# Performance work log

Hardware: AMD Instinct MI355X
Metric: run time of the kernel (lower is better)

Reference implementation:

```python
import jax, jax.numpy as jnp
import numpy as np

B, T, N = 32, 512, 16
C, V, D, H, L = 150, 832, 512, 512, 5  # chord vocab, note vocab, embed dim, hidden, layers


def setup_inputs() -> dict:
    key = jax.random.key(0)
    ks = jax.random.split(key, 16)
    s = 0.05
    note = jax.random.randint(ks[0], (B, T, N), 0, V)
    chord = jax.random.randint(ks[1], (B, T), 0, C)
    chord_table = jax.random.normal(ks[2], (C, D), jnp.float32) * s
    note_table = jax.random.normal(ks[3], (V, D), jnp.float32) * s
    # GRU layer 0 (input = 2*D), layers 1..L-1 (input = H), gate order r,z,n like torch
    w_ih0 = jax.random.normal(ks[4], (3 * H, 2 * D), jnp.float32) * s
    w_hh0 = jax.random.normal(ks[5], (3 * H, H), jnp.float32) * s
    b_ih0 = jax.random.normal(ks[6], (3 * H,), jnp.float32) * s
    b_hh0 = jax.random.normal(ks[7], (3 * H,), jnp.float32) * s
    w_ih_r = jax.random.normal(ks[8], (L - 1, 3 * H, H), jnp.float32) * s
    w_hh_r = jax.random.normal(ks[9], (L - 1, 3 * H, H), jnp.float32) * s
    b_ih_r = jax.random.normal(ks[10], (L - 1, 3 * H), jnp.float32) * s
    b_hh_r = jax.random.normal(ks[11], (L - 1, 3 * H), jnp.float32) * s
    fc_w = jax.random.normal(ks[12], (C, H), jnp.float32) * s
    fc_b = jax.random.normal(ks[13], (C,), jnp.float32) * s
    return dict(note=note, chord=chord, chord_table=chord_table, note_table=note_table,
                w_ih0=w_ih0, w_hh0=w_hh0, b_ih0=b_ih0, b_hh0=b_hh0,
                w_ih_r=w_ih_r, w_hh_r=w_hh_r, b_ih_r=b_ih_r, b_hh_r=b_hh_r,
                fc_w=fc_w, fc_b=fc_b)


def _gru_layer(x, wih, whh, bih, bhh):
    # x: [B, T, in] -> [B, T, H], torch GRU cell math (gate order r,z,n)
    xp = jnp.einsum('bti,gi->btg', x, wih) + bih          # precompute input proj [B,T,3H]
    xp = jnp.swapaxes(xp, 0, 1)                            # [T,B,3H]
    h0 = jnp.zeros((x.shape[0], whh.shape[1]), x.dtype)

    def step(h, xpt):
        gh = h @ whh.T + bhh
        xr, xz, xn = jnp.split(xpt, 3, axis=-1)
        hr, hz, hn = jnp.split(gh, 3, axis=-1)
        r = jax.nn.sigmoid(xr + hr)
        z = jax.nn.sigmoid(xz + hz)
        n = jnp.tanh(xn + r * hn)
        h_new = (1.0 - z) * n + z * h
        return h_new, h_new

    _, ys = jax.lax.scan(step, h0, xp)
    return jnp.swapaxes(ys, 0, 1)                          # [B,T,H]


def _forward(note, chord, chord_table, note_table, w_ih0, w_hh0, b_ih0, b_hh0,
             w_ih_r, w_hh_r, b_ih_r, b_hh_r, fc_w, fc_b):
    # padding_idx=0: zero row 0 of both tables (also blocks its gradient)
    ct = chord_table.at[0].set(0.0)
    nt = note_table.at[0].set(0.0)
    chord_emb = ct[chord]                                   # [B,T,D]
    # ragged mean over notes before first zero; mask[k]=1 iff no zero in note[...,:k+1]
    mask = jnp.cumprod((note != 0).astype(chord_table.dtype), axis=-1)  # [B,T,N]
    emb = nt[note]                                          # [B,T,N,D]
    cnt = jnp.maximum(mask.sum(-1), 1.0)                    # zero_index==0 case -> mean of zero row
    note_emb = jnp.einsum('btnd,btn->btd', emb, mask) / cnt[..., None]
    x = jnp.concatenate([chord_emb, note_emb], axis=-1)     # [B,T,2D]
    x = _gru_layer(x, w_ih0, w_hh0, b_ih0, b_hh0)
    for l in range(w_ih_r.shape[0]):
        x = _gru_layer(x, w_ih_r[l], w_hh_r[l], b_ih_r[l], b_hh_r[l])
    return x @ fc_w.T + fc_b                                # [B,T,C]


def reference(note, chord, chord_table, note_table, w_ih0, w_hh0, b_ih0, b_hh0,
              w_ih_r, w_hh_r, b_ih_r, b_hh_r, fc_w, fc_b):
    return _forward(note, chord, chord_table, note_table, w_ih0, w_hh0, b_ih0, b_hh0,
                    w_ih_r, w_hh_r, b_ih_r, b_hh_r, fc_w, fc_b)
```

## Files before the change

kernel.cpp:

```cpp
#include <hip/hip_runtime.h>
#include <hip/hip_bf16.h>

#define B_   32
#define T_   512
#define NN_  16
#define CV_  150
#define D_   512
#define H_   512
#define BT_  16384
#define K0_  1024
#define G3H_ 1536
#define SUBS_ 32
#define NBF_ 160
#define WSZ_ 49152

using bf16x8 = __attribute__((ext_vector_type(8))) short;
using f32x4  = __attribute__((ext_vector_type(4))) float;
using u32x4  = __attribute__((ext_vector_type(4))) unsigned int;
typedef unsigned long long u64;

__device__ __forceinline__ unsigned short f2bf(float f){
  unsigned int u = __builtin_bit_cast(unsigned int, f);
  u += 0x7fffu + ((u >> 16) & 1u);
  return (unsigned short)(u >> 16);
}

__device__ __forceinline__ void store8(unsigned short* p, f32x4 a, f32x4 b){
  union { unsigned short us[8]; u32x4 v; } u;
  u.us[0]=f2bf(a[0]); u.us[1]=f2bf(a[1]); u.us[2]=f2bf(a[2]); u.us[3]=f2bf(a[3]);
  u.us[4]=f2bf(b[0]); u.us[5]=f2bf(b[1]); u.us[6]=f2bf(b[2]); u.us[7]=f2bf(b[3]);
  *(u32x4*)p = u.v;
}

__device__ __forceinline__ u64 ld_coh_u64(const u64* p){
  return __hip_atomic_load(p, __ATOMIC_RELAXED, __HIP_MEMORY_SCOPE_AGENT);
}
__device__ __forceinline__ void st_coh_u32(void* p, unsigned int v){
  __hip_atomic_store((unsigned int*)p, v, __ATOMIC_RELAXED, __HIP_MEMORY_SCOPE_AGENT);
}
__device__ __forceinline__ void st_flag(int* p, int v){
  __hip_atomic_store(p, v, __ATOMIC_RELAXED, __HIP_MEMORY_SCOPE_AGENT);
}
__device__ __forceinline__ int ld_flag(const int* p){
  return __hip_atomic_load(p, __ATOMIC_RELAXED, __HIP_MEMORY_SCOPE_AGENT);
}

__global__ void convert_bf16(const float* __restrict__ src,
                             unsigned short* __restrict__ dst, int n){
  int i = blockIdx.x * 256 + threadIdx.x;
  if (i < n) dst[i] = f2bf(src[i]);
}

__global__ void prep_wfrag(const float* __restrict__ whh0,
                           const float* __restrict__ whhr,
                           const float* __restrict__ wihr,
                           unsigned short* __restrict__ wsw, int total){
  int idx = blockIdx.x * 256 + threadIdx.x;
  if (idx >= total) return;
  int pos = idx & 511;
  int lam = pos >> 3, e = pos & 7;
  int fr  = idx >> 9;
  int ks  = fr & 31;
  int g   = (fr >> 5) % 3;
  int blk = fr / 96;
  int sub = blk & 31, l = blk >> 5;
  int row = g * 512 + sub * 16 + (lam & 15);
  int k   = (ks & 15) * 32 + (lam >> 4) * 8 + e;
  float v;
  if (l == 0) v = (ks < 16) ? whh0[(size_t)row * H_ + k] : 0.f;
  else {
    const float* w = (ks < 16) ? (whhr + (size_t)(l - 1) * G3H_ * H_)
                               : (wihr + (size_t)(l - 1) * G3H_ * H_);
    v = w[(size_t)row * H_ + k];
  }
  wsw[idx] = f2bf(v);
}

__global__ void prep_bias(const float* __restrict__ bhh0,
                          const float* __restrict__ bihr,
                          const float* __restrict__ bhhr,
                          float* __restrict__ bias_sw, int total){
  int idx = blockIdx.x * 256 + threadIdx.x;
  if (idx >= total) return;
  int q = idx & 3, u = (idx >> 2) & 15, sub = (idx >> 6) & 31, l = idx >> 11;
  int j = sub * 16 + u;
  float v;
  if (l == 0){
    v = (q == 0) ? bhh0[j] : (q == 1) ? bhh0[512 + j] : (q == 2) ? 0.f : bhh0[1024 + j];
  } else {
    const float* bi = bihr + (size_t)(l - 1) * G3H_;
    const float* bh = bhhr + (size_t)(l - 1) * G3H_;
    v = (q == 0) ? bi[j] + bh[j]
      : (q == 1) ? bi[512 + j] + bh[512 + j]
      : (q == 2) ? bi[1024 + j] : bh[1024 + j];
  }
  bias_sw[idx] = v;
}

__global__ __launch_bounds__(64) void emb_kernel(
    const int* __restrict__ note, const int* __restrict__ chord,
    const float* __restrict__ ctab, const float* __restrict__ ntab,
    unsigned short* __restrict__ x0){
  const int bt = blockIdx.x;
  const int tid = threadIdx.x;
  __shared__ int sn[NN_];
  if (tid < NN_) sn[tid] = note[bt * NN_ + tid];
  __syncthreads();
  float alive = 1.f, cnt = 0.f;
  float msk[NN_];
  #pragma unroll
  for (int k = 0; k < NN_; ++k){ if (sn[k] == 0) alive = 0.f; msk[k] = alive; cnt += alive; }
  const float inv = 1.f / fmaxf(cnt, 1.f);
  const int ch = chord[bt];
  const int d0 = tid * 8;
  f32x4 c0 = {0.f,0.f,0.f,0.f}, c1 = {0.f,0.f,0.f,0.f};
  if (ch != 0){
    const float* cp = ctab + (size_t)ch * D_ + d0;
    c0 = *(const f32x4*)cp; c1 = *(const f32x4*)(cp + 4);
  }
  f32x4 s0 = {0.f,0.f,0.f,0.f}, s1 = {0.f,0.f,0.f,0.f};
  #pragma unroll
  for (int k = 0; k < NN_; ++k){
    if (msk[k] != 0.f){
      const float* np = ntab + (size_t)sn[k] * D_ + d0;
      s0 += *(const f32x4*)np;
      s1 += *(const f32x4*)(np + 4);
    }
  }
  s0 *= inv; s1 *= inv;
  unsigned short* o = x0 + (size_t)bt * K0_ + d0;
  store8(o, c0, c1);
  store8(o + D_, s0, s1);
}

__global__ __launch_bounds__(256) void gemm_bt(
    const unsigned short* __restrict__ X, const unsigned short* __restrict__ W,
    const float* __restrict__ bias, float* __restrict__ Y,
    int M, int N, int K, int wmode){
  const int lane = threadIdx.x & 63;
  const int wave = threadIdx.x >> 6;
  const int l15 = lane & 15, kq4 = lane >> 4;
  const int m_frag = blockIdx.y * 64 + wave * 16 + l15;
  const int n_base = blockIdx.x * 64;
  f32x4 acc[4] = {{0.f,0.f,0.f,0.f},{0.f,0.f,0.f,0.f},{0.f,0.f,0.f,0.f},{0.f,0.f,0.f,0.f}};
  const unsigned short* xptr = X + (size_t)m_frag * K + kq4 * 8;
  const unsigned short* wptr[4];
  #pragma unroll
  for (int i = 0; i < 4; ++i){
    int n = n_base + i * 16 + l15;
    if (n >= N) n = N - 1;
    wptr[i] = W + (size_t)n * K + kq4 * 8;
  }
  for (int k0 = 0; k0 < K; k0 += 32){
    bf16x8 a = *(const bf16x8*)(xptr + k0);
    #pragma unroll
    for (int i = 0; i < 4; ++i){
      bf16x8 b = *(const bf16x8*)(wptr[i] + k0);
      acc[i] = __builtin_amdgcn_mfma_f32_16x16x32_bf16(a, b, acc[i], 0, 0, 0);
    }
  }
  const int mrow = blockIdx.y * 64 + wave * 16 + kq4 * 4;
  #pragma unroll
  for (int i = 0; i < 4; ++i){
    int n = n_base + i * 16 + l15;
    if (n < N){
      float bv = bias[n];
      #pragma unroll
      for (int r = 0; r < 4; ++r){
        int m = mrow + r;
        float v = acc[i][r] + bv;
        if (wmode == 0) Y[(size_t)m * N + n] = v;
        else            Y[((size_t)(m & (T_-1)) * N + n) * B_ + (m >> 9)] = v;
      }
    }
  }
}

__global__ __launch_bounds__(256, 1) void gru_fused(
    const float* __restrict__ xp, const unsigned short* __restrict__ wsw,
    const float* __restrict__ bias_sw, unsigned short* __restrict__ hT,
    unsigned short* __restrict__ xT, unsigned short* __restrict__ xout,
    int* __restrict__ flags){
  __shared__ unsigned short w_s[96 * 512];
  __shared__ unsigned short stage_s[32 * 512];
  __shared__ float p_s[4][2][16][16];
  __shared__ float bias_s[64];

  const int tid = threadIdx.x;
  const int blk = blockIdx.x;
  const int l   = blk >> 5;
  const int sub = blk & 31;
  const int lane = tid & 63, wave = tid >> 6;
  const int l15 = lane & 15, l4 = lane >> 4;
  const int myn = wave >> 1;
  const bool rzw = (wave & 1) == 0;

  {
    const u32x4* src = (const u32x4*)(wsw + (size_t)blk * WSZ_);
    u32x4* dst = (u32x4*)w_s;
    #pragma unroll
    for (int i = 0; i < 24; ++i) dst[tid + 256 * i] = src[tid + 256 * i];
  }
  if (tid < 64) bias_s[tid] = bias_sw[blk * 64 + tid];

  const int cb = tid & 31;
  const int cj = (tid >> 5) * 2;
  const int jg = sub * 16 + cj;
  float hres0 = 0.f, hres1 = 0.f;

  unsigned short* hTl = hT + (size_t)l * (2 * 32 * 512);
  unsigned short* xTw = xT + (size_t)l * (4 * 32 * 512);
  const unsigned short* xTr = xT + (size_t)(l - 1) * (4 * 32 * 512);

  auto stage = [&](const unsigned short* __restrict__ src){
    u64 lo[8], hi[8];
    #pragma unroll
    for (int i = 0; i < 8; ++i){
      int c = tid + 256 * i;
      int f = c >> 6, lam = c & 63;
      int b = ((f >> 4) << 4) | (lam & 15);
      int k = ((f & 15) << 5) | ((lam >> 4) << 3);
      const u64* sp = (const u64*)(src + b * 512 + k);
      lo[i] = ld_coh_u64(sp);
      hi[i] = ld_coh_u64(sp + 1);
    }
    #pragma unroll
    for (int i = 0; i < 8; ++i){
      int c = tid + 256 * i;
      *(u64*)&stage_s[c * 8]     = lo[i];
      *(u64*)&stage_s[c * 8 + 4] = hi[i];
    }
  };

  __syncthreads();

  for (int s = 0; s < T_ + 4; ++s){
    const int t = s - l;
    const bool act = (t >= 0) && (t < T_);
    if (act){
      f32x4 accA = {0.f,0.f,0.f,0.f}, accB = {0.f,0.f,0.f,0.f};
      stage(hTl + (size_t)(t & 1) * (32 * 512));
      __syncthreads();
      #pragma unroll
      for (int ks = 0; ks < 16; ++ks){
        bf16x8 b = *(const bf16x8*)&stage_s[((myn << 4) + ks) * 512 + lane * 8];
        if (rzw){
          bf16x8 a0 = *(const bf16x8*)&w_s[(0 * 32 + ks) * 512 + lane * 8];
          bf16x8 a1 = *(const bf16x8*)&w_s[(1 * 32 + ks) * 512 + lane * 8];
          accA = __builtin_amdgcn_mfma_f32_16x16x32_bf16(a0, b, accA, 0, 0, 0);
          accB = __builtin_amdgcn_mfma_f32_16x16x32_bf16(a1, b, accB, 0, 0, 0);
        } else {
          bf16x8 a2 = *(const bf16x8*)&w_s[(2 * 32 + ks) * 512 + lane * 8];
          accA = __builtin_amdgcn_mfma_f32_16x16x32_bf16(a2, b, accA, 0, 0, 0);
        }
      }
      float er = 0.f, ez = 0.f, en = 0.f, er1 = 0.f, ez1 = 0.f, en1 = 0.f;
      if (l > 0){
        __syncthreads();
        stage(xTr + (size_t)(t & 3) * (32 * 512));
        __syncthreads();
        #pragma unroll
        for (int ks = 0; ks < 16; ++ks){
          bf16x8 b = *(const bf16x8*)&stage_s[((myn << 4) + ks) * 512 + lane * 8];
          if (rzw){
            bf16x8 a0 = *(const bf16x8*)&w_s[(0 * 32 + 16 + ks) * 512 + lane * 8];
            bf16x8 a1 = *(const bf16x8*)&w_s[(1 * 32 + 16 + ks) * 512 + lane * 8];
            accA = __builtin_amdgcn_mfma_f32_16x16x32_bf16(a0, b, accA, 0, 0, 0);
            accB = __builtin_amdgcn_mfma_f32_16x16x32_bf16(a1, b, accB, 0, 0, 0);
          } else {
            bf16x8 a2 = *(const bf16x8*)&w_s[(2 * 32 + 16 + ks) * 512 + lane * 8];
            accB = __builtin_amdgcn_mfma_f32_16x16x32_bf16(a2, b, accB, 0, 0, 0);
          }
        }
      } else {
        const float* xb = xp + (size_t)t * (G3H_ * B_) + cb;
        er  = xb[(size_t)(0 * H_ + jg) * B_];  er1 = xb[(size_t)(0 * H_ + jg + 1) * B_];
        ez  = xb[(size_t)(1 * H_ + jg) * B_];  ez1 = xb[(size_t)(1 * H_ + jg + 1) * B_];
        en  = xb[(size_t)(2 * H_ + jg) * B_];  en1 = xb[(size_t)(2 * H_ + jg + 1) * B_];
      }
      #pragma unroll
      for (int r = 0; r < 4; ++r){
        int u = l4 * 4 + r;
        if (rzw){ p_s[0][myn][u][l15] = accA[r]; p_s[1][myn][u][l15] = accB[r]; }
        else    { p_s[2][myn][u][l15] = accA[r]; p_s[3][myn][u][l15] = accB[r]; }
      }
      __syncthreads();
      {
        const int nt = cb >> 4, bc = cb & 15;
        const float* bs = bias_s + cj * 4;
        float rp0 = p_s[0][nt][cj][bc],     rp1 = p_s[0][nt][cj + 1][bc];
        float zp0 = p_s[1][nt][cj][bc],     zp1 = p_s[1][nt][cj + 1][bc];
        float hp0 = p_s[2][nt][cj][bc],     hp1 = p_s[2][nt][cj + 1][bc];
        float xq0 = p_s[3][nt][cj][bc],     xq1 = p_s[3][nt][cj + 1][bc];
        float r0 = 1.f / (1.f + __expf(-(rp0 + er  + bs[0])));
        float r1 = 1.f / (1.f + __expf(-(rp1 + er1 + bs[4])));
        float z0 = 1.f / (1.f + __expf(-(zp0 + ez  + bs[1])));
        float z1 = 1.f / (1.f + __expf(-(zp1 + ez1 + bs[5])));
        float nx0 = (l > 0) ? (xq0 + bs[2]) : en;
        float nx1 = (l > 0) ? (xq1 + bs[6]) : en1;
        float e0 = __expf(2.f * (nx0 + r0 * (hp0 + bs[3])));
        float e1 = __expf(2.f * (nx1 + r1 * (hp1 + bs[7])));
        float n0 = (e0 - 1.f) / (e0 + 1.f);
        float n1 = (e1 - 1.f) / (e1 + 1.f);
        float h0 = (1.f - z0) * n0 + z0 * hres0; hres0 = h0;
        float h1 = (1.f - z1) * n1 + z1 * hres1; hres1 = h1;
        unsigned int pk = (unsigned int)f2bf(h0) | ((unsigned int)f2bf(h1) << 16);
        st_coh_u32(hTl + (size_t)((t + 1) & 1) * (32 * 512) + cb * 512 + jg, pk);
        if (l < 4) st_coh_u32(xTw + (size_t)(t & 3) * (32 * 512) + cb * 512 + jg, pk);
        else *(unsigned int*)&xout[((size_t)cb * T_ + t) * H_ + jg] = pk;
      }
    }
    __syncthreads();
    if (tid == 0) st_flag(&flags[blk], s + 1);
    if (tid < 64){
      const int tgt = s + 1;
      while (true){
        int v0 = ld_flag(&flags[tid]);
        int v1 = ld_flag(&flags[tid + 64]);
        int v2 = (tid < 32) ? ld_flag(&flags[tid + 128]) : tgt;
        if (__all(v0 >= tgt && v1 >= tgt && v2 >= tgt)) break;
      }
    }
    __syncthreads();
  }
}

extern "C" void kernel_launch(void* const* d_in, const int* in_sizes, int n_in,
                              void* d_out, int out_size, void* d_ws, size_t ws_size,
                              hipStream_t stream){
  (void)in_sizes; (void)n_in; (void)out_size; (void)ws_size;
  const int*   note  = (const int*)d_in[0];
  const int*   chord = (const int*)d_in[1];
  const float* ctab  = (const float*)d_in[2];
  const float* ntab  = (const float*)d_in[3];
  const float* wih0  = (const float*)d_in[4];
  const float* whh0  = (const float*)d_in[5];
  const float* bih0  = (const float*)d_in[6];
  const float* bhh0  = (const float*)d_in[7];
  const float* wihr  = (const float*)d_in[8];
  const float* whhr  = (const float*)d_in[9];
  const float* bihr  = (const float*)d_in[10];
  const float* bhhr  = (const float*)d_in[11];
  const float* fcw   = (const float*)d_in[12];
  const float* fcb   = (const float*)d_in[13];
  float* out = (float*)d_out;

  char* ws = (char*)d_ws;
  size_t off = 0;
  auto alloc = [&](size_t bytes)->char*{
    char* p = ws + off; off = (off + bytes + 255) & ~(size_t)255; return p;
  };
  int*            flags   = (int*)alloc((size_t)NBF_ * sizeof(int));
  float*          xp      = (float*)alloc((size_t)BT_ * G3H_ * 4);
  unsigned short* x0      = (unsigned short*)alloc((size_t)BT_ * K0_ * 2);
  unsigned short* xout    = (unsigned short*)alloc((size_t)BT_ * H_ * 2);
  unsigned short* hT      = (unsigned short*)alloc((size_t)5 * 2 * 32 * 512 * 2);
  unsigned short* xT      = (unsigned short*)alloc((size_t)4 * 4 * 32 * 512 * 2);
  unsigned short* wsw     = (unsigned short*)alloc((size_t)NBF_ * WSZ_ * 2);
  float*          bias_sw = (float*)alloc((size_t)NBF_ * 64 * 4);
  unsigned short* wih0_b  = (unsigned short*)alloc((size_t)G3H_ * K0_ * 2);
  unsigned short* fcw_b   = (unsigned short*)alloc((size_t)CV_ * H_ * 2);

  hipMemsetAsync(flags, 0, (size_t)NBF_ * sizeof(int), stream);
  hipMemsetAsync(hT, 0, (size_t)5 * 2 * 32 * 512 * 2, stream);

  { int n = G3H_ * K0_; convert_bf16<<<(n + 255) / 256, 256, 0, stream>>>(wih0, wih0_b, n); }
  { int n = CV_ * H_;   convert_bf16<<<(n + 255) / 256, 256, 0, stream>>>(fcw, fcw_b, n); }
  { int n = NBF_ * WSZ_;
    prep_wfrag<<<(n + 255) / 256, 256, 0, stream>>>(whh0, whhr, wihr, wsw, n); }
  { int n = NBF_ * 64;
    prep_bias<<<(n + 255) / 256, 256, 0, stream>>>(bhh0, bihr, bhhr, bias_sw, n); }

  emb_kernel<<<BT_, 64, 0, stream>>>(note, chord, ctab, ntab, x0);

  gemm_bt<<<dim3(G3H_ / 64, BT_ / 64), 256, 0, stream>>>(x0, wih0_b, bih0, xp, BT_, G3H_, K0_, 1);

  gru_fused<<<NBF_, 256, 0, stream>>>(xp, wsw, bias_sw, hT, xT, xout, flags);

  gemm_bt<<<dim3((CV_ + 63) / 64, BT_ / 64), 256, 0, stream>>>(
      xout, fcw_b, fcb, out, BT_, CV_, H_, 0);
}
```

Before: 6.382 ms.

## Replace global lockstep barrier with per-layer producer/consumer flags in fused GRU

The single global barrier across all 160 blocks at every wavefront step is replaced by per-layer flag arrays. Each block now waits only on its own layer's blocks for the previous timestep, the previous layer's blocks for the current input, and the next layer's blocks for ring-buffer slack of up to 3 steps. Layers can then run decoupled instead of in rigid lockstep. The layer input fragments are also loaded straight from global into registers rather than staged through shared memory, and biases are moved into registers, which removes two block syncs per step. The risk lies in the correctness of the ring-buffer depth and flag targets, and in higher register pressure.

```diff
diff --git a/kernel.cpp b/kernel.cpp
--- a/kernel.cpp
+++ b/kernel.cpp
@@ -184,7 +184,6 @@
   __shared__ unsigned short w_s[96 * 512];
   __shared__ unsigned short stage_s[32 * 512];
   __shared__ float p_s[4][2][16][16];
-  __shared__ float bias_s[64];
 
   const int tid = threadIdx.x;
   const int blk = blockIdx.x;
@@ -201,127 +200,146 @@
     #pragma unroll
     for (int i = 0; i < 24; ++i) dst[tid + 256 * i] = src[tid + 256 * i];
   }
-  if (tid < 64) bias_s[tid] = bias_sw[blk * 64 + tid];
 
   const int cb = tid & 31;
   const int cj = (tid >> 5) * 2;
   const int jg = sub * 16 + cj;
+  const float* bsp = bias_sw + blk * 64;
+  const float br0 = bsp[cj*4+0],     bz0 = bsp[cj*4+1],     bx0 = bsp[cj*4+2],     bn0 = bsp[cj*4+3];
+  const float br1 = bsp[(cj+1)*4+0], bz1 = bsp[(cj+1)*4+1], bx1 = bsp[(cj+1)*4+2], bn1 = bsp[(cj+1)*4+3];
   float hres0 = 0.f, hres1 = 0.f;
 
   unsigned short* hTl = hT + (size_t)l * (2 * 32 * 512);
   unsigned short* xTw = xT + (size_t)l * (4 * 32 * 512);
   const unsigned short* xTr = xT + (size_t)(l - 1) * (4 * 32 * 512);
-
-  auto stage = [&](const unsigned short* __restrict__ src){
-    u64 lo[8], hi[8];
-    #pragma unroll
-    for (int i = 0; i < 8; ++i){
-      int c = tid + 256 * i;
-      int f = c >> 6, lam = c & 63;
-      int b = ((f >> 4) << 4) | (lam & 15);
-      int k = ((f & 15) << 5) | ((lam >> 4) << 3);
-      const u64* sp = (const u64*)(src + b * 512 + k);
-      lo[i] = ld_coh_u64(sp);
-      hi[i] = ld_coh_u64(sp + 1);
-    }
-    #pragma unroll
-    for (int i = 0; i < 8; ++i){
-      int c = tid + 256 * i;
-      *(u64*)&stage_s[c * 8]     = lo[i];
-      *(u64*)&stage_s[c * 8 + 4] = hi[i];
-    }
-  };
+  int*       fl_own  = flags + l * 64;
+  const int* fl_prod = flags + (l > 0 ? (l - 1) * 64 : l * 64);
+  const int* fl_cons = flags + (l + 1) * 64;
 
   __syncthreads();
 
-  for (int s = 0; s < T_ + 4; ++s){
-    const int t = s - l;
-    const bool act = (t >= 0) && (t < T_);
-    if (act){
-      f32x4 accA = {0.f,0.f,0.f,0.f}, accB = {0.f,0.f,0.f,0.f};
-      stage(hTl + (size_t)(t & 1) * (32 * 512));
-      __syncthreads();
+  for (int t = 0; t < T_; ++t){
+    if (wave == 0){
+      const int* pp; int tgt;
+      if (lane < 32){ pp = fl_own + lane; tgt = t; }
+      else if (l > 0){ pp = fl_prod + (lane - 32); tgt = t + 1; }
+      else { pp = fl_own + (lane - 32); tgt = -(1 << 30); }
+      while (true){ int v = ld_flag(pp); if (__all(v >= tgt)) break; }
+    } else if (wave == 1 && l < 4){
+      const int* pp = fl_cons + (lane & 31);
+      const int tgt = t - 3;
+      while (true){
+        int v = (lane < 32) ? ld_flag(pp) : 0x7fffffff;
+        if (__all(v >= tgt)) break;
+      }
+    }
+    __syncthreads();
+
+    float er = 0.f, ez = 0.f, en = 0.f, er1 = 0.f, ez1 = 0.f, en1 = 0.f;
+    if (l == 0){
+      const float* xb = xp + (size_t)t * (G3H_ * B_) + cb;
+      er  = xb[(size_t)(0 * H_ + jg) * B_];  er1 = xb[(size_t)(0 * H_ + jg + 1) * B_];
+      ez  = xb[(size_t)(1 * H_ + jg) * B_];  ez1 = xb[(size_t)(1 * H_ + jg + 1) * B_];
+      en  = xb[(size_t)(2 * H_ + jg) * B_];  en1 = xb[(size_t)(2 * H_ + jg + 1) * B_];
+    }
+
+    {
+      const unsigned short* hsrc = hTl + (size_t)(t & 1) * (32 * 512);
+      u64 lo[8], hi[8];
+      #pragma unroll
+      for (int i = 0; i < 8; ++i){
+        int c = tid + 256 * i;
+        int f = c >> 6, lam = c & 63;
+        int b = ((f >> 4) << 4) | (lam & 15);
+        int k = ((f & 15) << 5) | ((lam >> 4) << 3);
+        const u64* sp = (const u64*)(hsrc + b * 512 + k);
+        lo[i] = ld_coh_u64(sp);
+        hi[i] = ld_coh_u64(sp + 1);
+      }
+      #pragma unroll
+      for (int i = 0; i < 8; ++i){
+        int c = tid + 256 * i;
+        *(u64*)&stage_s[c * 8]     = lo[i];
+        *(u64*)&stage_s[c * 8 + 4] = hi[i];
+      }
+    }
+
+    union Ufrag { u64 q[2]; bf16x8 v; };
+    Ufrag xb[16];
+    if (l > 0){
+      const unsigned short* xs = xTr + (size_t)(t & 3) * (32 * 512)
+                               + (size_t)(myn * 16 + l15) * 512 + l4 * 8;
       #pragma unroll
       for (int ks = 0; ks < 16; ++ks){
-        bf16x8 b = *(const bf16x8*)&stage_s[((myn << 4) + ks) * 512 + lane * 8];
+        const u64* sp = (const u64*)(xs + ks * 32);
+        xb[ks].q[0] = ld_coh_u64(sp);
+        xb[ks].q[1] = ld_coh_u64(sp + 1);
+      }
+    }
+    __syncthreads();
+
+    f32x4 accA = {0.f,0.f,0.f,0.f}, accB = {0.f,0.f,0.f,0.f};
+    #pragma unroll
+    for (int ks = 0; ks < 16; ++ks){
+      bf16x8 b = *(const bf16x8*)&stage_s[((myn << 4) + ks) * 512 + lane * 8];
+      if (rzw){
+        bf16x8 a0 = *(const bf16x8*)&w_s[(0 * 32 + ks) * 512 + lane * 8];
+        bf16x8 a1 = *(const bf16x8*)&w_s[(1 * 32 + ks) * 512 + lane * 8];
+        accA = __builtin_amdgcn_mfma_f32_16x16x32_bf16(a0, b, accA, 0, 0, 0);
+        accB = __builtin_amdgcn_mfma_f32_16x16x32_bf16(a1, b, accB, 0, 0, 0);
+      } else {
+        bf16x8 a2 = *(const bf16x8*)&w_s[(2 * 32 + ks) * 512 + lane * 8];
+        accA = __builtin_amdgcn_mfma_f32_16x16x32_bf16(a2, b, accA, 0, 0, 0);
+      }
+    }
+    if (l > 0){
+      #pragma unroll
+      for (int ks = 0; ks < 16; ++ks){
+        bf16x8 b = xb[ks].v;
         if (rzw){
-          bf16x8 a0 = *(const bf16x8*)&w_s[(0 * 32 + ks) * 512 + lane * 8];
-          bf16x8 a1 = *(const bf16x8*)&w_s[(1 * 32 + ks) * 512 + lane * 8];
+          bf16x8 a0 = *(const bf16x8*)&w_s[(0 * 32 + 16 + ks) * 512 + lane * 8];
+          bf16x8 a1 = *(const bf16x8*)&w_s[(1 * 32 + 16 + ks) * 512 + lane * 8];
           accA = __builtin_amdgcn_mfma_f32_16x16x32_bf16(a0, b, accA, 0, 0, 0);
           accB = __builtin_amdgcn_mfma_f32_16x16x32_bf16(a1, b, accB, 0, 0, 0);
         } else {
-          bf16x8 a2 = *(const bf16x8*)&w_s[(2 * 32 + ks) * 512 + lane * 8];
-          accA = __builtin_amdgcn_mfma_f32_16x16x32_bf16(a2, b, accA, 0, 0, 0);
+          bf16x8 a2 = *(const bf16x8*)&w_s[(2 * 32 + 16 + ks) * 512 + lane * 8];
+          accB = __builtin_amdgcn_mfma_f32_16x16x32_bf16(a2, b, accB, 0, 0, 0);
         }
       }
-      float er = 0.f, ez = 0.f, en = 0.f, er1 = 0.f, ez1 = 0.f, en1 = 0.f;
-      if (l > 0){
-        __syncthreads();
-        stage(xTr + (size_t)(t & 3) * (32 * 512));
-        __syncthreads();
-        #pragma unroll
-        for (int ks = 0; ks < 16; ++ks){
-          bf16x8 b = *(const bf16x8*)&stage_s[((myn << 4) + ks) * 512 + lane * 8];
-          if (rzw){
-            bf16x8 a0 = *(const bf16x8*)&w_s[(0 * 32 + 16 + ks) * 512 + lane * 8];
-            bf16x8 a1 = *(const bf16x8*)&w_s[(1 * 32 + 16 + ks) * 512 + lane * 8];
-            accA = __builtin_amdgcn_mfma_f32_16x16x32_bf16(a0, b, accA, 0, 0, 0);
-            accB = __builtin_amdgcn_mfma_f32_16x16x32_bf16(a1, b, accB, 0, 0, 0);
-          } else {
-            bf16x8 a2 = *(const bf16x8*)&w_s[(2 * 32 + 16 + ks) * 512 + lane * 8];
-            accB = __builtin_amdgcn_mfma_f32_16x16x32_bf16(a2, b, accB, 0, 0, 0);
-          }
-        }
-      } else {
-        const float* xb = xp + (size_t)t * (G3H_ * B_) + cb;
-        er  = xb[(size_t)(0 * H_ + jg) * B_];  er1 = xb[(size_t)(0 * H_ + jg + 1) * B_];
-        ez  = xb[(size_t)(1 * H_ + jg) * B_];  ez1 = xb[(size_t)(1 * H_ + jg + 1) * B_];
-        en  = xb[(size_t)(2 * H_ + jg) * B_];  en1 = xb[(size_t)(2 * H_ + jg + 1) * B_];
-      }
-      #pragma unroll
-      for (int r = 0; r < 4; ++r){
-        int u = l4 * 4 + r;
-        if (rzw){ p_s[0][myn][u][l15] = accA[r]; p_s[1][myn][u][l15] = accB[r]; }
-        else    { p_s[2][myn][u][l15] = accA[r]; p_s[3][myn][u][l15] = accB[r]; }
-      }
-      __syncthreads();
-      {
-        const int nt = cb >> 4, bc = cb & 15;
-        const float* bs = bias_s + cj * 4;
-        float rp0 = p_s[0][nt][cj][bc],     rp1 = p_s[0][nt][cj + 1][bc];
-        float zp0 = p_s[1][nt][cj][bc],     zp1 = p_s[1][nt][cj + 1][bc];
-        float hp0 = p_s[2][nt][cj][bc],     hp1 = p_s[2][nt][cj + 1][bc];
-        float xq0 = p_s[3][nt][cj][bc],     xq1 = p_s[3][nt][cj + 1][bc];
-        float r0 = 1.f / (1.f + __expf(-(rp0 + er  + bs[0])));
-        float r1 = 1.f / (1.f + __expf(-(rp1 + er1 + bs[4])));
-        float z0 = 1.f / (1.f + __expf(-(zp0 + ez  + bs[1])));
-        float z1 = 1.f / (1.f + __expf(-(zp1 + ez1 + bs[5])));
-        float nx0 = (l > 0) ? (xq0 + bs[2]) : en;
-        float nx1 = (l > 0) ? (xq1 + bs[6]) : en1;
-        float e0 = __expf(2.f * (nx0 + r0 * (hp0 + bs[3])));
-        float e1 = __expf(2.f * (nx1 + r1 * (hp1 + bs[7])));
-        float n0 = (e0 - 1.f) / (e0 + 1.f);
-        float n1 = (e1 - 1.f) / (e1 + 1.f);
-        float h0 = (1.f - z0) * n0 + z0 * hres0; hres0 = h0;
-        float h1 = (1.f - z1) * n1 + z1 * hres1; hres1 = h1;
-        unsigned int pk = (unsigned int)f2bf(h0) | ((unsigned int)f2bf(h1) << 16);
-        st_coh_u32(hTl + (size_t)((t + 1) & 1) * (32 * 512) + cb * 512 + jg, pk);
-        if (l < 4) st_coh_u32(xTw + (size_t)(t & 3) * (32 * 512) + cb * 512 + jg, pk);
-        else *(unsigned int*)&xout[((size_t)cb * T_ + t) * H_ + jg] = pk;
-      }
+    }
+    #pragma unroll
+    for (int r = 0; r < 4; ++r){
+      int u = l4 * 4 + r;
+      if (rzw){ p_s[0][myn][u][l15] = accA[r]; p_s[1][myn][u][l15] = accB[r]; }
+      else    { p_s[2][myn][u][l15] = accA[r]; p_s[3][myn][u][l15] = accB[r]; }
     }
     __syncthreads();
-    if (tid == 0) st_flag(&flags[blk], s + 1);
-    if (tid < 64){
-      const int tgt = s + 1;
-      while (true){
-        int v0 = ld_flag(&flags[tid]);
-        int v1 = ld_flag(&flags[tid + 64]);
-        int v2 = (tid < 32) ? ld_flag(&flags[tid + 128]) : tgt;
-        if (__all(v0 >= tgt && v1 >= tgt && v2 >= tgt)) break;
-      }
+
+    {
+      const int nt = cb >> 4, bc = cb & 15;
+      float rp0 = p_s[0][nt][cj][bc],     rp1 = p_s[0][nt][cj + 1][bc];
+      float zp0 = p_s[1][nt][cj][bc],     zp1 = p_s[1][nt][cj + 1][bc];
+      float hp0 = p_s[2][nt][cj][bc],     hp1 = p_s[2][nt][cj + 1][bc];
+      float xq0 = p_s[3][nt][cj][bc],     xq1 = p_s[3][nt][cj + 1][bc];
+      float r0 = 1.f / (1.f + __expf(-(rp0 + er  + br0)));
+      float r1 = 1.f / (1.f + __expf(-(rp1 + er1 + br1)));
+      float z0 = 1.f / (1.f + __expf(-(zp0 + ez  + bz0)));
+      float z1 = 1.f / (1.f + __expf(-(zp1 + ez1 + bz1)));
+      float nx0 = (l > 0) ? (xq0 + bx0) : en;
+      float nx1 = (l > 0) ? (xq1 + bx1) : en1;
+      float e0 = __expf(2.f * (nx0 + r0 * (hp0 + bn0)));
+      float e1 = __expf(2.f * (nx1 + r1 * (hp1 + bn1)));
+      float n0 = (e0 - 1.f) / (e0 + 1.f);
+      float n1 = (e1 - 1.f) / (e1 + 1.f);
+      float h0 = (1.f - z0) * n0 + z0 * hres0; hres0 = h0;
+      float h1 = (1.f - z1) * n1 + z1 * hres1; hres1 = h1;
+      unsigned int pk = (unsigned int)f2bf(h0) | ((unsigned int)f2bf(h1) << 16);
+      st_coh_u32(hTl + (size_t)((t + 1) & 1) * (32 * 512) + cb * 512 + jg, pk);
+      if (l < 4) st_coh_u32(xTw + (size_t)(t & 3) * (32 * 512) + cb * 512 + jg, pk);
+      else *(unsigned int*)&xout[((size_t)cb * T_ + t) * H_ + jg] = pk;
     }
     __syncthreads();
+    if (tid == 0) st_flag(fl_own + sub, t + 1);
   }
 }
 
@@ -350,7 +368,7 @@
   auto alloc = [&](size_t bytes)->char*{
     char* p = ws + off; off = (off + bytes + 255) & ~(size_t)255; return p;
   };
-  int*            flags   = (int*)alloc((size_t)NBF_ * sizeof(int));
+  int*            flags   = (int*)alloc((size_t)5 * 64 * sizeof(int));
   float*          xp      = (float*)alloc((size_t)BT_ * G3H_ * 4);
   unsigned short* x0      = (unsigned short*)alloc((size_t)BT_ * K0_ * 2);
   unsigned short* xout    = (unsigned short*)alloc((size_t)BT_ * H_ * 2);
@@ -361,7 +379,7 @@
   unsigned short* wih0_b  = (unsigned short*)alloc((size_t)G3H_ * K0_ * 2);
   unsigned short* fcw_b   = (unsigned short*)alloc((size_t)CV_ * H_ * 2);
 
-  hipMemsetAsync(flags, 0, (size_t)NBF_ * sizeof(int), stream);
+  hipMemsetAsync(flags, 0, (size_t)5 * 64 * sizeof(int), stream);
   hipMemsetAsync(hT, 0, (size_t)5 * 2 * 32 * 512 * 2, stream);
 
   { int n = G3H_ * K0_; convert_bf16<<<(n + 255) / 256, 256, 0, stream>>>(wih0, wih0_b, n); }
```

After: 6.090 ms. 4.6% less time.
